# Kernel optimization log

Measured on AMD Instinct MI355X. Metric: run time of the kernel, lower is better.

The kernel has to match this reference:

```python
import jax, jax.numpy as jnp
import numpy as np

CH = 16        # channel_n
HID = 128      # hidden_size
IN_CH = 3      # input_channels (locked each step)
FIRE_RATE = 0.5


def _dwconv3x3(x, w, b):
    # depthwise 3x3, reflect padding (torch padding_mode='reflect', padding=1)
    xp = jnp.pad(x, ((0, 0), (0, 0), (1, 1), (1, 1)), mode='reflect')
    y = jax.lax.conv_general_dilated(
        xp, w, window_strides=(1, 1), padding='VALID',
        dimension_numbers=('NCHW', 'OIHW', 'NCHW'), feature_group_count=CH)
    return y + b[None, :, None, None]


def _conv1x1(x, w, b=None):
    # w: (out_ch, in_ch) -- squeezed 1x1 conv kernel
    y = jnp.einsum('bchw,oc->bohw', x, w)
    return y if b is None else y + b[None, :, None, None]


def setup_inputs() -> dict:
    key = jax.random.key(0)
    ks = jax.random.split(key, 8)
    B, H, W = 4, 256, 256
    x = jax.random.normal(ks[0], (B, CH, H, W), dtype=jnp.float32)
    # depthwise kernels: (CH, 1, 3, 3)
    p0_w = jax.random.normal(ks[1], (CH, 1, 3, 3), dtype=jnp.float32) * (1.0 / 3.0)
    p0_b = jax.random.normal(ks[2], (CH,), dtype=jnp.float32) * 0.1
    p1_w = jax.random.normal(ks[3], (CH, 1, 3, 3), dtype=jnp.float32) * (1.0 / 3.0)
    p1_b = jax.random.normal(ks[4], (CH,), dtype=jnp.float32) * 0.1
    # fc0: Conv2d(3*CH -> HID, k=1); fc1: Conv2d(HID -> CH, k=1, bias=False)
    fc0_w = jax.random.normal(ks[5], (HID, 3 * CH), dtype=jnp.float32) * (1.0 / np.sqrt(3 * CH))
    fc0_b = jax.random.normal(ks[6], (HID,), dtype=jnp.float32) * 0.1
    # NOTE: torch zero-inits fc1; we use small random weights so the reference is non-trivial.
    fc1_w = jax.random.normal(ks[7], (CH, HID), dtype=jnp.float32) * (0.1 / np.sqrt(HID))
    return {"x": x, "p0_w": p0_w, "p0_b": p0_b, "p1_w": p1_w, "p1_b": p1_b,
            "fc0_w": fc0_w, "fc0_b": fc0_b, "fc1_w": fc1_w, "steps": 32}


def reference(x, p0_w, p0_b, p1_w, p1_b, fc0_w, fc0_b, fc1_w, steps):
    B, _, H, W = x.shape
    input_image = x[:, :IN_CH]  # clone of input channels, re-written each step
    keys = jax.random.split(jax.random.key(42), steps)

    @jax.checkpoint
    def step(x, key):
        # perceive: depthwise 3x3 x2, concat with state
        z1 = _dwconv3x3(x, p0_w, p0_b)
        z2 = _dwconv3x3(x, p1_w, p1_b)
        y = jnp.concatenate([x, z1, z2], axis=1)        # [B, 3*CH, H, W]
        # 1x1-conv MLP
        dx = jax.nn.relu(_conv1x1(y, fc0_w, fc0_b))      # [B, HID, H, W]
        dx = _conv1x1(dx, fc1_w)                         # [B, CH, H, W]
        # stochastic fire mask: rand > fire_rate, broadcast over channels
        mask = (jax.random.uniform(key, (B, 1, H, W), dtype=x.dtype) > FIRE_RATE).astype(x.dtype)
        x = x + dx * mask                                # residual update
        x = x.at[:, :IN_CH].set(input_image)             # channel lock
        return x, None

    x, _ = jax.lax.scan(step, x, keys)
    out = x[:, 3]  # segmentation channel
    return out, x
```

## Files before the change

kernel.cpp:

```cpp
#include <hip/hip_runtime.h>
#include <cstdint>

#define CH     16
#define HPIX   256
#define WPIX   256
#define BATCH  4
#define HID    128
#define STEPS  32
#define PLANE  (HPIX * WPIX)
#define MASK_N (BATCH * PLANE)

#define TW 16
#define TH 8
#define XTW 18
#define XTH 10
#define NPX (XTH * XTW)
#define HSF 20

typedef _Float16 half8  __attribute__((ext_vector_type(8)));
typedef _Float16 half4e __attribute__((ext_vector_type(4)));
typedef float floatx4  __attribute__((ext_vector_type(4)));
typedef float floatx16 __attribute__((ext_vector_type(16)));

__host__ __device__ static inline void tf2x32(uint32_t k0, uint32_t k1,
                                              uint32_t x0, uint32_t x1,
                                              uint32_t& o0, uint32_t& o1) {
  const uint32_t ks2 = k0 ^ k1 ^ 0x1BD11BDAu;
#define TFROT(a) { x0 += x1; x1 = (x1 << (a)) | (x1 >> (32 - (a))); x1 ^= x0; }
  x0 += k0;  x1 += k1;
  TFROT(13) TFROT(15) TFROT(26) TFROT(6)
  x0 += k1;  x1 += ks2 + 1u;
  TFROT(17) TFROT(29) TFROT(16) TFROT(24)
  x0 += ks2; x1 += k0 + 2u;
  TFROT(13) TFROT(15) TFROT(26) TFROT(6)
  x0 += k0;  x1 += k1 + 3u;
  TFROT(17) TFROT(29) TFROT(16) TFROT(24)
  x0 += k1;  x1 += ks2 + 4u;
  TFROT(13) TFROT(15) TFROT(26) TFROT(6)
  x0 += ks2; x1 += k0 + 5u;
#undef TFROT
  o0 = x0; o1 = x1;
}

__device__ __forceinline__ int refl(int v) {
  return v < 0 ? -v : (v > HPIX - 1 ? 2 * (HPIX - 1) - v : v);
}

__global__ __launch_bounds__(256) void prep_weights(
    const float* __restrict__ fc0_w, const float* __restrict__ fc0_b,
    const float* __restrict__ fc1_w,
    const float* __restrict__ p0_w, const float* __restrict__ p0_b,
    const float* __restrict__ p1_w, const float* __restrict__ p1_b,
    _Float16* __restrict__ Mh, _Float16* __restrict__ W1h,
    float* __restrict__ bp) {
  const int idx = blockIdx.x * 256 + threadIdx.x;
  if (idx < 9 * HID * CH) {
    const int tap = idx / (HID * CH);
    const int rem = idx - tap * (HID * CH);
    const int h = rem >> 4, c = rem & 15;
    float m = fc0_w[h * 48 + 16 + c] * p0_w[c * 9 + tap]
            + fc0_w[h * 48 + 32 + c] * p1_w[c * 9 + tap];
    if (tap == 4) m += fc0_w[h * 48 + c];
    Mh[(tap * HID + h) * CH + c] = (_Float16)m;
  } else if (idx < 9 * HID * CH + CH * HID) {
    const int i2 = idx - 9 * HID * CH;
    W1h[i2] = (_Float16)fc1_w[i2];
  } else if (idx < 9 * HID * CH + CH * HID + HID) {
    const int h = idx - (9 * HID * CH + CH * HID);
    float s = fc0_b[h];
    for (int c = 0; c < CH; ++c)
      s += fc0_w[h * 48 + 16 + c] * p0_b[c]
         + fc0_w[h * 48 + 32 + c] * p1_b[c];
    bp[h] = s;
  }
}

__global__ __launch_bounds__(256) void init_state(
    const float* __restrict__ x, _Float16* __restrict__ S) {
  const int i = blockIdx.x * 256 + threadIdx.x;
  const int b = i >> 16;
  const int p = i & (PLANE - 1);
  const float* __restrict__ xp = x + (size_t)b * CH * PLANE + p;
  half8 lo, hi;
  #pragma unroll
  for (int c = 0; c < 8; ++c) lo[c] = (_Float16)xp[(size_t)c * PLANE];
  #pragma unroll
  for (int c = 0; c < 8; ++c) hi[c] = (_Float16)xp[(size_t)(c + 8) * PLANE];
  _Float16* d = S + (size_t)i * CH;
  *(half8*)(d)     = lo;
  *(half8*)(d + 8) = hi;
}

__global__ __launch_bounds__(256) void nca_step(
    const _Float16* __restrict__ s_in, _Float16* __restrict__ s_out,
    const float* __restrict__ x0,
    const _Float16* __restrict__ Mh, const _Float16* __restrict__ W1h,
    const float* __restrict__ bp,
    uint32_t k0, uint32_t k1, int wrgb,
    float* __restrict__ xfinal, float* __restrict__ outp) {
  __shared__ __align__(16) _Float16 halo[NPX * HSF];
  __shared__ __align__(16) _Float16 Hbuf[64 * HID];
  __shared__ float maskbuf[128];

  const int tid = threadIdx.x;
  const int w0 = blockIdx.x * TW;
  const int h0 = blockIdx.y * TH;
  const int b  = blockIdx.z;

  const int wv   = tid >> 6;
  const int lane = tid & 63;
  const int n    = lane & 15;
  const int g    = lane >> 4;
  const int c32  = lane & 31;
  const int q2   = lane >> 5;

  half8 Atap[9];
  #pragma unroll
  for (int t = 0; t < 9; ++t)
    Atap[t] = *(const half8*)(Mh + ((t * HID + 32 * wv + c32) << 4) + 8 * q2);
  half8 bw1[4];
  #pragma unroll
  for (int s = 0; s < 4; ++s)
    bw1[s] = *(const half8*)(W1h + n * HID + 32 * s + 8 * g);
  float4 bias4[4];
  #pragma unroll
  for (int rb = 0; rb < 4; ++rb)
    bias4[rb] = *(const float4*)(bp + 32 * wv + 8 * rb + 4 * q2);

  if (tid < NPX) {
    const int hr = tid / XTW, hc = tid - (tid / XTW) * XTW;
    const int gh = refl(h0 + hr - 1);
    const int gw = refl(w0 + hc - 1);
    const uint4* __restrict__ sp = (const uint4*)(
        s_in + ((size_t)b * PLANE + (size_t)gh * WPIX + gw) * CH);
    const uint4 va = sp[0];
    const uint4 vb = sp[1];
    uint32_t* hd = (uint32_t*)(halo + tid * HSF);
    hd[0] = va.x; hd[1] = va.y; hd[2] = va.z; hd[3] = va.w;
    hd[4] = vb.x; hd[5] = vb.y; hd[6] = vb.z; hd[7] = vb.w;
  }

  if (tid < 128) {
    const int tr = tid >> 4, tc = tid & 15;
    const uint32_t j = (uint32_t)(b * PLANE + (h0 + tr) * WPIX + (w0 + tc));
    uint32_t r0, r1;
    tf2x32(k0, k1, 0u, j, r0, r1);
    const uint32_t bits = r0 ^ r1;
    union { uint32_t i; float f; } cvt;
    cvt.i = (bits >> 9) | 0x3F800000u;
    maskbuf[tid] = ((cvt.f - 1.0f) > 0.5f) ? 1.0f : 0.0f;
  }
  __syncthreads();

  const float* __restrict__ x0b = x0 + (size_t)b * CH * PLANE;

  #pragma unroll
  for (int half = 0; half < 2; ++half) {
    #pragma unroll
    for (int cti = 0; cti < 2; ++cti) {
      const int ct   = 2 * half + cti;
      const int prow = 2 * ct + (c32 >> 4);
      const int pcol = c32 & 15;
      half8 btap[9];
      #pragma unroll
      for (int dr = 0; dr < 3; ++dr) {
        #pragma unroll
        for (int dj = 0; dj < 3; ++dj) {
          const _Float16* hp =
              halo + ((prow + dr) * XTW + pcol + dj) * HSF + 8 * q2;
          const half4e lo = *(const half4e*)hp;
          const half4e hi = *(const half4e*)(hp + 4);
          half8 ff;
          ff[0] = lo[0]; ff[1] = lo[1]; ff[2] = lo[2]; ff[3] = lo[3];
          ff[4] = hi[0]; ff[5] = hi[1]; ff[6] = hi[2]; ff[7] = hi[3];
          btap[dr * 3 + dj] = ff;
        }
      }
      floatx16 acc = {0.f,0.f,0.f,0.f,0.f,0.f,0.f,0.f,
                      0.f,0.f,0.f,0.f,0.f,0.f,0.f,0.f};
      #pragma unroll
      for (int t = 0; t < 9; ++t)
        acc = __builtin_amdgcn_mfma_f32_32x32x16_f16(Atap[t], btap[t], acc,
                                                     0, 0, 0);
      const int px  = 32 * ct + c32;
      const int ph  = px & 63;
      const int n16 = px & 15;
      #pragma unroll
      for (int rb = 0; rb < 4; ++rb) {
        half4e hv;
        hv[0] = (_Float16)fmaxf(acc[4 * rb + 0] + bias4[rb].x, 0.f);
        hv[1] = (_Float16)fmaxf(acc[4 * rb + 1] + bias4[rb].y, 0.f);
        hv[2] = (_Float16)fmaxf(acc[4 * rb + 2] + bias4[rb].z, 0.f);
        hv[3] = (_Float16)fmaxf(acc[4 * rb + 3] + bias4[rb].w, 0.f);
        *(half4e*)(Hbuf + ph * HID + (((4 * wv + rb) ^ n16) << 3) + 4 * q2) = hv;
      }
    }
    __syncthreads();

    {
      const int ct2 = 4 * half + wv;
      floatx4 c2 = {0.f, 0.f, 0.f, 0.f};
      #pragma unroll
      for (int ks = 0; ks < 4; ++ks) {
        const half8 a2 = *(const half8*)(
            Hbuf + (16 * (ct2 & 3) + n) * HID + (((4 * ks + g) ^ n) << 3));
        c2 = __builtin_amdgcn_mfma_f32_16x16x32_f16(a2, bw1[ks], c2, 0, 0, 0);
      }
      const float4 mk = *(const float4*)(maskbuf + 16 * ct2 + 4 * g);
      const float mka[4] = {mk.x, mk.y, mk.z, mk.w};
      const int hb = ((ct2 + 1) * XTW + 4 * g + 1) * HSF + n;
      float r[4];
      #pragma unroll
      for (int e = 0; e < 4; ++e) {
        const float bx = (float)halo[hb + e * HSF];
        r[e] = (n < 3) ? bx : fmaf(mka[e], c2[e], bx);
      }
      _Float16* dp = s_out
          + ((size_t)b * PLANE + (size_t)(h0 + ct2) * WPIX + w0 + 4 * g) * CH
          + n;
      dp[0 * CH] = (_Float16)r[0];
      dp[1 * CH] = (_Float16)r[1];
      dp[2 * CH] = (_Float16)r[2];
      dp[3 * CH] = (_Float16)r[3];
      if (wrgb) {
        const size_t xoff = (size_t)n * PLANE
                          + (size_t)(h0 + ct2) * WPIX + w0 + 4 * g;
        float4 o;
        if (n < 3) o = *(const float4*)(x0b + xoff);
        else { o.x = r[0]; o.y = r[1]; o.z = r[2]; o.w = r[3]; }
        *(float4*)(xfinal + (size_t)b * CH * PLANE + xoff) = o;
        if (n == 3)
          *(float4*)(outp + (size_t)b * PLANE
                     + (size_t)(h0 + ct2) * WPIX + w0 + 4 * g) = o;
      }
    }
    if (half == 0) __syncthreads();
  }
}

extern "C" void kernel_launch(void* const* d_in, const int* in_sizes, int n_in,
                              void* d_out, int out_size, void* d_ws, size_t ws_size,
                              hipStream_t stream) {
  const float* x     = (const float*)d_in[0];
  const float* p0_w  = (const float*)d_in[1];
  const float* p0_b  = (const float*)d_in[2];
  const float* p1_w  = (const float*)d_in[3];
  const float* p1_b  = (const float*)d_in[4];
  const float* fc0_w = (const float*)d_in[5];
  const float* fc0_b = (const float*)d_in[6];
  const float* fc1_w = (const float*)d_in[7];

  uint32_t kk[STEPS][2];
  for (int i = 0; i < STEPS; ++i) {
    uint32_t a, b2;
    tf2x32(0u, 42u, 0u, (uint32_t)i, a, b2);
    kk[i][0] = a;
    kk[i][1] = b2;
  }

  float* out    = (float*)d_out;
  float* xfinal = out + MASK_N;

  _Float16* Mh  = (_Float16*)((char*)d_ws + ((size_t)32 << 20));
  _Float16* W1h = Mh + 9 * HID * CH;
  float*    bpr = (float*)((char*)W1h + CH * HID * 2);
  _Float16* S0  = (_Float16*)((char*)d_ws + ((size_t)40 << 20));
  _Float16* S1  = (_Float16*)((char*)d_ws + ((size_t)56 << 20));

  const int prep_n = 9 * HID * CH + CH * HID + HID;
  prep_weights<<<dim3((prep_n + 255) / 256), dim3(256), 0, stream>>>(
      fc0_w, fc0_b, fc1_w, p0_w, p0_b, p1_w, p1_b, Mh, W1h, bpr);
  init_state<<<dim3(MASK_N / 256), dim3(256), 0, stream>>>(x, S0);

  const dim3 grid(WPIX / TW, HPIX / TH, BATCH);
  const dim3 block(256);

  for (int i = 0; i < STEPS; ++i) {
    const _Float16* src = (i & 1) ? S1 : S0;
    _Float16*       dst = (i & 1) ? S0 : S1;
    nca_step<<<grid, block, 0, stream>>>(src, dst, x, Mh, W1h, bpr,
                                         kk[i][0], kk[i][1],
                                         (i == STEPS - 1) ? 1 : 0,
                                         xfinal, out);
  }
}
```

Baseline: 691.6 us.

## Split work by pixel per wave instead of hidden channel, removing block syncs

Each wave now owns 32 pixels and loops over all four 32-channel hidden slices, reloading the fc0 tap weights each iteration, instead of owning one hidden slice for all pixels. The hidden activations stay in a private per-wave region of shared memory, so the two mid-kernel __syncthreads are gone and the fc1 stage reads only the wave's own data. The change also adds a launch-bounds occupancy hint of 4 blocks per CU. In exchange, shared memory for the hidden buffer doubles, and the A-operand weights are fetched from global or cache four times per wave rather than once.

```diff
diff --git a/kernel.cpp b/kernel.cpp
--- a/kernel.cpp
+++ b/kernel.cpp
@@ -91,7 +91,7 @@
   *(half8*)(d + 8) = hi;
 }
 
-__global__ __launch_bounds__(256) void nca_step(
+__global__ __launch_bounds__(256, 4) void nca_step(
     const _Float16* __restrict__ s_in, _Float16* __restrict__ s_out,
     const float* __restrict__ x0,
     const _Float16* __restrict__ Mh, const _Float16* __restrict__ W1h,
@@ -99,7 +99,7 @@
     uint32_t k0, uint32_t k1, int wrgb,
     float* __restrict__ xfinal, float* __restrict__ outp) {
   __shared__ __align__(16) _Float16 halo[NPX * HSF];
-  __shared__ __align__(16) _Float16 Hbuf[64 * HID];
+  __shared__ __align__(16) _Float16 Hbuf[4 * 32 * HID];
   __shared__ float maskbuf[128];
 
   const int tid = threadIdx.x;
@@ -114,18 +114,10 @@
   const int c32  = lane & 31;
   const int q2   = lane >> 5;
 
-  half8 Atap[9];
-  #pragma unroll
-  for (int t = 0; t < 9; ++t)
-    Atap[t] = *(const half8*)(Mh + ((t * HID + 32 * wv + c32) << 4) + 8 * q2);
   half8 bw1[4];
   #pragma unroll
   for (int s = 0; s < 4; ++s)
     bw1[s] = *(const half8*)(W1h + n * HID + 32 * s + 8 * g);
-  float4 bias4[4];
-  #pragma unroll
-  for (int rb = 0; rb < 4; ++rb)
-    bias4[rb] = *(const float4*)(bp + 32 * wv + 8 * rb + 4 * q2);
 
   if (tid < NPX) {
     const int hr = tid / XTW, hc = tid - (tid / XTW) * XTW;
@@ -152,89 +144,92 @@
   }
   __syncthreads();
 
+  const int prow = 2 * wv + (c32 >> 4);
+  const int pcol = c32 & 15;
+  half8 btap[9];
+  #pragma unroll
+  for (int dr = 0; dr < 3; ++dr) {
+    #pragma unroll
+    for (int dj = 0; dj < 3; ++dj) {
+      const _Float16* hp =
+          halo + ((prow + dr) * XTW + pcol + dj) * HSF + 8 * q2;
+      const half4e lo = *(const half4e*)hp;
+      const half4e hi = *(const half4e*)(hp + 4);
+      half8 ff;
+      ff[0] = lo[0]; ff[1] = lo[1]; ff[2] = lo[2]; ff[3] = lo[3];
+      ff[4] = hi[0]; ff[5] = hi[1]; ff[6] = hi[2]; ff[7] = hi[3];
+      btap[dr * 3 + dj] = ff;
+    }
+  }
+
+  _Float16* __restrict__ Hw = Hbuf + (wv << 12);
+  const int n16 = c32 & 15;
+
+  #pragma unroll 1
+  for (int m = 0; m < 4; ++m) {
+    half8 Atap[9];
+    #pragma unroll
+    for (int t = 0; t < 9; ++t)
+      Atap[t] = *(const half8*)(Mh + ((t * HID + 32 * m + c32) << 4) + 8 * q2);
+    float4 bias4[4];
+    #pragma unroll
+    for (int rb = 0; rb < 4; ++rb)
+      bias4[rb] = *(const float4*)(bp + 32 * m + 8 * rb + 4 * q2);
+    floatx16 acc = {0.f,0.f,0.f,0.f,0.f,0.f,0.f,0.f,
+                    0.f,0.f,0.f,0.f,0.f,0.f,0.f,0.f};
+    #pragma unroll
+    for (int t = 0; t < 9; ++t)
+      acc = __builtin_amdgcn_mfma_f32_32x32x16_f16(Atap[t], btap[t], acc,
+                                                   0, 0, 0);
+    #pragma unroll
+    for (int rb = 0; rb < 4; ++rb) {
+      half4e hv;
+      hv[0] = (_Float16)fmaxf(acc[4 * rb + 0] + bias4[rb].x, 0.f);
+      hv[1] = (_Float16)fmaxf(acc[4 * rb + 1] + bias4[rb].y, 0.f);
+      hv[2] = (_Float16)fmaxf(acc[4 * rb + 2] + bias4[rb].z, 0.f);
+      hv[3] = (_Float16)fmaxf(acc[4 * rb + 3] + bias4[rb].w, 0.f);
+      *(half4e*)(Hw + c32 * HID + (((4 * m + rb) ^ n16) << 3) + 4 * q2) = hv;
+    }
+  }
+
   const float* __restrict__ x0b = x0 + (size_t)b * CH * PLANE;
-
-  #pragma unroll
-  for (int half = 0; half < 2; ++half) {
-    #pragma unroll
-    for (int cti = 0; cti < 2; ++cti) {
-      const int ct   = 2 * half + cti;
-      const int prow = 2 * ct + (c32 >> 4);
-      const int pcol = c32 & 15;
-      half8 btap[9];
-      #pragma unroll
-      for (int dr = 0; dr < 3; ++dr) {
-        #pragma unroll
-        for (int dj = 0; dj < 3; ++dj) {
-          const _Float16* hp =
-              halo + ((prow + dr) * XTW + pcol + dj) * HSF + 8 * q2;
-          const half4e lo = *(const half4e*)hp;
-          const half4e hi = *(const half4e*)(hp + 4);
-          half8 ff;
-          ff[0] = lo[0]; ff[1] = lo[1]; ff[2] = lo[2]; ff[3] = lo[3];
-          ff[4] = hi[0]; ff[5] = hi[1]; ff[6] = hi[2]; ff[7] = hi[3];
-          btap[dr * 3 + dj] = ff;
-        }
-      }
-      floatx16 acc = {0.f,0.f,0.f,0.f,0.f,0.f,0.f,0.f,
-                      0.f,0.f,0.f,0.f,0.f,0.f,0.f,0.f};
-      #pragma unroll
-      for (int t = 0; t < 9; ++t)
-        acc = __builtin_amdgcn_mfma_f32_32x32x16_f16(Atap[t], btap[t], acc,
-                                                     0, 0, 0);
-      const int px  = 32 * ct + c32;
-      const int ph  = px & 63;
-      const int n16 = px & 15;
-      #pragma unroll
-      for (int rb = 0; rb < 4; ++rb) {
-        half4e hv;
-        hv[0] = (_Float16)fmaxf(acc[4 * rb + 0] + bias4[rb].x, 0.f);
-        hv[1] = (_Float16)fmaxf(acc[4 * rb + 1] + bias4[rb].y, 0.f);
-        hv[2] = (_Float16)fmaxf(acc[4 * rb + 2] + bias4[rb].z, 0.f);
-        hv[3] = (_Float16)fmaxf(acc[4 * rb + 3] + bias4[rb].w, 0.f);
-        *(half4e*)(Hbuf + ph * HID + (((4 * wv + rb) ^ n16) << 3) + 4 * q2) = hv;
-      }
-    }
-    __syncthreads();
-
-    {
-      const int ct2 = 4 * half + wv;
-      floatx4 c2 = {0.f, 0.f, 0.f, 0.f};
-      #pragma unroll
-      for (int ks = 0; ks < 4; ++ks) {
-        const half8 a2 = *(const half8*)(
-            Hbuf + (16 * (ct2 & 3) + n) * HID + (((4 * ks + g) ^ n) << 3));
-        c2 = __builtin_amdgcn_mfma_f32_16x16x32_f16(a2, bw1[ks], c2, 0, 0, 0);
-      }
-      const float4 mk = *(const float4*)(maskbuf + 16 * ct2 + 4 * g);
-      const float mka[4] = {mk.x, mk.y, mk.z, mk.w};
-      const int hb = ((ct2 + 1) * XTW + 4 * g + 1) * HSF + n;
-      float r[4];
-      #pragma unroll
-      for (int e = 0; e < 4; ++e) {
-        const float bx = (float)halo[hb + e * HSF];
-        r[e] = (n < 3) ? bx : fmaf(mka[e], c2[e], bx);
-      }
-      _Float16* dp = s_out
-          + ((size_t)b * PLANE + (size_t)(h0 + ct2) * WPIX + w0 + 4 * g) * CH
-          + n;
-      dp[0 * CH] = (_Float16)r[0];
-      dp[1 * CH] = (_Float16)r[1];
-      dp[2 * CH] = (_Float16)r[2];
-      dp[3 * CH] = (_Float16)r[3];
-      if (wrgb) {
-        const size_t xoff = (size_t)n * PLANE
-                          + (size_t)(h0 + ct2) * WPIX + w0 + 4 * g;
-        float4 o;
-        if (n < 3) o = *(const float4*)(x0b + xoff);
-        else { o.x = r[0]; o.y = r[1]; o.z = r[2]; o.w = r[3]; }
-        *(float4*)(xfinal + (size_t)b * CH * PLANE + xoff) = o;
-        if (n == 3)
-          *(float4*)(outp + (size_t)b * PLANE
-                     + (size_t)(h0 + ct2) * WPIX + w0 + 4 * g) = o;
-      }
-    }
-    if (half == 0) __syncthreads();
+  #pragma unroll
+  for (int t2 = 0; t2 < 2; ++t2) {
+    floatx4 c2 = {0.f, 0.f, 0.f, 0.f};
+    #pragma unroll
+    for (int ks = 0; ks < 4; ++ks) {
+      const half8 a2 = *(const half8*)(
+          Hw + (16 * t2 + n) * HID + (((4 * ks + g) ^ n) << 3));
+      c2 = __builtin_amdgcn_mfma_f32_16x16x32_f16(a2, bw1[ks], c2, 0, 0, 0);
+    }
+    const int ct2 = 2 * wv + t2;
+    const float4 mk = *(const float4*)(maskbuf + 16 * ct2 + 4 * g);
+    const float mka[4] = {mk.x, mk.y, mk.z, mk.w};
+    const int hb = ((ct2 + 1) * XTW + 4 * g + 1) * HSF + n;
+    float r[4];
+    #pragma unroll
+    for (int e = 0; e < 4; ++e) {
+      const float bx = (float)halo[hb + e * HSF];
+      r[e] = (n < 3) ? bx : fmaf(mka[e], c2[e], bx);
+    }
+    _Float16* dp = s_out
+        + ((size_t)b * PLANE + (size_t)(h0 + ct2) * WPIX + w0 + 4 * g) * CH
+        + n;
+    dp[0 * CH] = (_Float16)r[0];
+    dp[1 * CH] = (_Float16)r[1];
+    dp[2 * CH] = (_Float16)r[2];
+    dp[3 * CH] = (_Float16)r[3];
+    if (wrgb) {
+      const size_t xoff = (size_t)n * PLANE
+                        + (size_t)(h0 + ct2) * WPIX + w0 + 4 * g;
+      float4 o;
+      if (n < 3) o = *(const float4*)(x0b + xoff);
+      else { o.x = r[0]; o.y = r[1]; o.z = r[2]; o.w = r[3]; }
+      *(float4*)(xfinal + (size_t)b * CH * PLANE + xoff) = o;
+      if (n == 3)
+        *(float4*)(outp + (size_t)b * PLANE
+                   + (size_t)(h0 + ct2) * WPIX + w0 + 4 * g) = o;
+    }
   }
 }
 
```

After: 746.1 us. +7.9%, slower.
